# Performance work log

Hardware: AMD Instinct MI355X
Metric: run time of the kernel (lower is better)

## Reference

```python
import jax, jax.numpy as jnp
import numpy as np

INPUT_DIM = 512
OUTPUT_DIM = 512
DEGREE = 7
ALPHA = 0.5


def setup_inputs() -> dict:
    key = jax.random.key(0)
    kx, kc = jax.random.split(key)
    x = jax.random.normal(kx, (8192, INPUT_DIM), dtype=jnp.float32)
    std = 1.0 / (INPUT_DIM * (DEGREE + 1))
    laguerre_coeffs = jax.random.normal(kc, (INPUT_DIM, OUTPUT_DIM, DEGREE + 1), dtype=jnp.float32) * std
    return {"x": x, "laguerre_coeffs": laguerre_coeffs}


def reference(x, laguerre_coeffs):
    # x: [B, I] -> tanh squashed
    xt = jnp.tanh(x.reshape(-1, INPUT_DIM))
    # Build Laguerre basis L_0..L_degree via the standard recurrence:
    # k*L_k = (2(k-1)+1+alpha - x)*L_{k-1} - (k-1+alpha)*L_{k-2}
    L0 = jnp.ones_like(xt)
    basis = [L0]
    if DEGREE > 0:
        L1 = 1.0 + ALPHA - xt
        basis.append(L1)
        Lkm2, Lkm1 = L0, L1
        for k in range(2, DEGREE + 1):
            Lk = ((2 * (k - 1) + 1 + ALPHA - xt) * Lkm1 - (k - 1 + ALPHA) * Lkm2) / k
            basis.append(Lk)
            Lkm2, Lkm1 = Lkm1, Lk
    laguerre = jnp.stack(basis, axis=-1)  # [B, I, D+1]
    y = jnp.einsum('bid,iod->bo', laguerre, laguerre_coeffs)
    return y
```

## Files before the change

kernel.cpp:

```cpp
#include <hip/hip_runtime.h>

#define B_ROWS 8192
#define IN_DIM 512
#define OUT_DIM 512
#define NDEG 8
#define KDIM (IN_DIM * NDEG)
#define ZSLICES 4
#define NKT 16
#define BM 256
#define BN 128
#define LDB 72

typedef short bf16x8 __attribute__((ext_vector_type(8)));
typedef float f32x4  __attribute__((ext_vector_type(4)));

__device__ __forceinline__ unsigned short f2bf(float f) {
  unsigned u = __float_as_uint(f);
  u += 0x7fffu + ((u >> 16) & 1u);
  return (unsigned short)(u >> 16);
}

__device__ __forceinline__ void laguerre8(float t, float* L) {
  L[0] = 1.0f;
  L[1] = 1.5f - t;
#pragma unroll
  for (int k = 2; k < NDEG; ++k)
    L[k] = ((2.0f * (float)k - 0.5f - t) * L[k - 1] -
            ((float)k - 0.5f) * L[k - 2]) * (1.0f / (float)k);
}

__global__ void basis_kernel(const float* __restrict__ x, unsigned short* __restrict__ A) {
  int idx = blockIdx.x * 256 + threadIdx.x;
  int b = idx >> 9, i = idx & 511;
  float L[NDEG];
  laguerre8(tanhf(x[idx]), L);
  uint4 v;
  v.x = (unsigned)f2bf(L[0]) | ((unsigned)f2bf(L[1]) << 16);
  v.y = (unsigned)f2bf(L[2]) | ((unsigned)f2bf(L[3]) << 16);
  v.z = (unsigned)f2bf(L[4]) | ((unsigned)f2bf(L[5]) << 16);
  v.w = (unsigned)f2bf(L[6]) | ((unsigned)f2bf(L[7]) << 16);
  int T = b >> 8, r = b & 255, kt = i >> 3, c = i & 7;
  size_t chunk = ((size_t)(T * 64 + kt)) * 2048 + r * 8 + (c ^ (r & 7));
  ((uint4*)A)[chunk] = v;
}

__global__ void coeff_kernel(const float* __restrict__ c, unsigned short* __restrict__ Bt) {
  int idx = blockIdx.x * 256 + threadIdx.x;
  int i = idx >> 9, o = idx & 511;
  const float4* cp = (const float4*)(c + (size_t)idx * 8);
  float4 c0 = cp[0], c1 = cp[1];
  uint4 v;
  v.x = (unsigned)f2bf(c0.x) | ((unsigned)f2bf(c0.y) << 16);
  v.y = (unsigned)f2bf(c0.z) | ((unsigned)f2bf(c0.w) << 16);
  v.z = (unsigned)f2bf(c1.x) | ((unsigned)f2bf(c1.y) << 16);
  v.w = (unsigned)f2bf(c1.z) | ((unsigned)f2bf(c1.w) << 16);
  ((uint4*)Bt)[o * 512 + i] = v;
}

__global__ __launch_bounds__(512, 4) void gemm_kernel(const unsigned short* __restrict__ A,
                                                      const unsigned short* __restrict__ Bt,
                                                      unsigned short* __restrict__ P) {
  __shared__ unsigned short lds[32768];
  unsigned short* As = lds;
  unsigned short* Bs = lds + 16384;

  const int tid = threadIdx.x;
  const int lane = tid & 63;
  const int w = tid >> 6;
  const int wm = w >> 1, wn = w & 1;

  const int g = blockIdx.x;
  const int xcd = g & 7, idx = g >> 3;
  const int z = xcd >> 1;
  const int y = (xcd & 1) * 16 + (idx & 15);
  const int bn = (idx >> 4) * BN;

  const uint4* Ag = (const uint4*)A;
  const uint4* Bg = (const uint4*)Bt;
  const size_t tile0 = ((size_t)(y * 64 + z * NKT)) * 2048;

  const int rB = tid >> 2, cB = (tid & 3) * 2;
  uint4 rb0 = Bg[(size_t)(bn + rB) * 512 + z * NKT * 8 + cB];
  uint4 rb1 = Bg[(size_t)(bn + rB) * 512 + z * NKT * 8 + cB + 1];

  const int arow = lane & 15, hi = lane >> 4;
  const int swz0 = hi ^ (arow & 7);
  const unsigned short* a0 = As + (wm * 64 + arow) * 64 + swz0 * 8;
  const unsigned short* a1 = As + (wm * 64 + arow) * 64 + (swz0 ^ 4) * 8;
  const unsigned short* bb = Bs + (wn * 64 + arow) * LDB;

  f32x4 zero = {0.f, 0.f, 0.f, 0.f};
  f32x4 acc[4][4];
#pragma unroll
  for (int mi = 0; mi < 4; ++mi)
#pragma unroll
    for (int ni = 0; ni < 4; ++ni) acc[mi][ni] = zero;

  for (int kt = 0; kt < NKT; ++kt) {
    __syncthreads();
    {
      size_t base = tile0 + (size_t)kt * 2048 + w * 256;
#pragma unroll
      for (int j = 0; j < 4; ++j) {
        const uint4* gp = Ag + base + j * 64 + lane;
        __builtin_amdgcn_global_load_lds(
            (const __attribute__((address_space(1))) unsigned int*)gp,
            (__attribute__((address_space(3))) unsigned int*)(As + (w * 256 + j * 64) * 8),
            16, 0, 0);
      }
    }
    *(uint4*)&Bs[rB * LDB + cB * 8] = rb0;
    *(uint4*)&Bs[rB * LDB + (cB + 1) * 8] = rb1;
    __syncthreads();

    if (kt + 1 < NKT) {
      rb0 = Bg[(size_t)(bn + rB) * 512 + (z * NKT + kt + 1) * 8 + cB];
      rb1 = Bg[(size_t)(bn + rB) * 512 + (z * NKT + kt + 1) * 8 + cB + 1];
    }

#pragma unroll
    for (int ks = 0; ks < 2; ++ks) {
      const unsigned short* ap = ks ? a1 : a0;
      bf16x8 af[4], bfr[4];
#pragma unroll
      for (int mi = 0; mi < 4; ++mi)
        af[mi] = *(const bf16x8*)(ap + mi * 1024);
#pragma unroll
      for (int ni = 0; ni < 4; ++ni)
        bfr[ni] = *(const bf16x8*)(bb + ni * 16 * LDB + ks * 32 + hi * 8);
#pragma unroll
      for (int mi = 0; mi < 4; ++mi)
#pragma unroll
        for (int ni = 0; ni < 4; ++ni)
          acc[mi][ni] = __builtin_amdgcn_mfma_f32_16x16x32_bf16(af[mi], bfr[ni], acc[mi][ni], 0, 0, 0);
    }
  }

  __syncthreads();
  unsigned short* W = lds + w * 4096;
#pragma unroll
  for (int mi = 0; mi < 4; ++mi)
#pragma unroll
    for (int ni = 0; ni < 4; ++ni) {
      int col = ni * 16 + arow;
      int c8 = col >> 3, cpos = col & 7;
#pragma unroll
      for (int r = 0; r < 4; ++r) {
        int row = mi * 16 + hi * 4 + r;
        W[row * 64 + ((c8 ^ (row & 7)) << 3) + cpos] = f2bf(acc[mi][ni][r]);
      }
    }
  const int rr = lane >> 3, cc = lane & 7;
#pragma unroll
  for (int it = 0; it < 8; ++it) {
    int row = it * 8 + rr;
    uint4 v = *(uint4*)&W[row * 64 + ((cc ^ (row & 7)) << 3)];
    size_t pr = ((size_t)z * B_ROWS + (y * 256 + wm * 64 + row)) * 512 + bn + wn * 64 + cc * 8;
    *(uint4*)&P[pr] = v;
  }
}

__global__ void reduce_kernel(const unsigned short* __restrict__ P, float* __restrict__ out) {
  size_t t = (size_t)blockIdx.x * 256 + threadIdx.x;
  const uint4* p = (const uint4*)P;
  const size_t stride = (size_t)B_ROWS * OUT_DIM / 8;
  float s[8] = {0, 0, 0, 0, 0, 0, 0, 0};
#pragma unroll
  for (int zz = 0; zz < ZSLICES; ++zz) {
    uint4 v = p[t + zz * stride];
    unsigned q[4] = {v.x, v.y, v.z, v.w};
#pragma unroll
    for (int j = 0; j < 4; ++j) {
      s[2 * j]     += __uint_as_float((q[j] & 0xffffu) << 16);
      s[2 * j + 1] += __uint_as_float(q[j] & 0xffff0000u);
    }
  }
  float4 o0 = {s[0], s[1], s[2], s[3]}, o1 = {s[4], s[5], s[6], s[7]};
  ((float4*)out)[t * 2]     = o0;
  ((float4*)out)[t * 2 + 1] = o1;
}

__global__ void naive_kernel(const float* __restrict__ x, const float* __restrict__ c,
                             float* __restrict__ out) {
  __shared__ float bas[IN_DIM * NDEG];
  int b = blockIdx.x;
  for (int i = threadIdx.x; i < IN_DIM; i += 256) {
    float t = tanhf(x[(size_t)b * IN_DIM + i]);
    float L[NDEG];
    laguerre8(t, L);
#pragma unroll
    for (int d = 0; d < NDEG; ++d) bas[i * NDEG + d] = L[d];
  }
  __syncthreads();
  for (int o = threadIdx.x; o < OUT_DIM; o += 256) {
    float acc = 0.f;
    for (int i = 0; i < IN_DIM; ++i) {
      const float* cp = c + ((size_t)i * OUT_DIM + o) * NDEG;
#pragma unroll
      for (int d = 0; d < NDEG; ++d) acc += bas[i * NDEG + d] * cp[d];
    }
    out[(size_t)b * OUT_DIM + o] = acc;
  }
}

extern "C" void kernel_launch(void* const* d_in, const int* in_sizes, int n_in,
                              void* d_out, int out_size, void* d_ws, size_t ws_size,
                              hipStream_t stream) {
  const float* x    = (const float*)d_in[0];
  const float* coef = (const float*)d_in[1];
  float* out = (float*)d_out;

  const size_t A_BYTES  = (size_t)B_ROWS * KDIM * 2;
  const size_t P_BYTES  = (size_t)ZSLICES * B_ROWS * OUT_DIM * 2;
  const size_t BT_BYTES = (size_t)OUT_DIM * KDIM * 2;

  if (ws_size >= A_BYTES + P_BYTES + BT_BYTES) {
    unsigned short* Abuf = (unsigned short*)d_ws;
    unsigned short* Pp   = (unsigned short*)((char*)d_ws + A_BYTES);
    unsigned short* Bt   = (unsigned short*)((char*)d_ws + A_BYTES + P_BYTES);
    basis_kernel<<<(B_ROWS * IN_DIM) / 256, 256, 0, stream>>>(x, Abuf);
    coeff_kernel<<<(IN_DIM * OUT_DIM) / 256, 256, 0, stream>>>(coef, Bt);
    gemm_kernel<<<512, 512, 0, stream>>>(Abuf, Bt, Pp);
    reduce_kernel<<<(B_ROWS * OUT_DIM / 8) / 256, 256, 0, stream>>>(Pp, out);
  } else if (ws_size >= A_BYTES + BT_BYTES) {
    naive_kernel<<<B_ROWS, 256, 0, stream>>>(x, coef, out);
  } else {
    naive_kernel<<<B_ROWS, 256, 0, stream>>>(x, coef, out);
  }
}
```

Before: 73.22 us.

## Double-buffer GEMM LDS tiles and merge basis/coeff prep kernels

Merges the basis and coefficient conversion kernels into a single prep launch to save one kernel launch. Rewrites the GEMM main loop to double-buffer the A and B tiles in LDS, so the next tile's async global-to-LDS loads overlap the current tile's MFMAs, leaving one barrier per iteration. It also raises MFMA wave priority with s_setprio. LDS grows to 100KB and launch_bounds min blocks drop from 4 to 2, which may cut occupancy.

```diff
diff --git a/kernel.cpp b/kernel.cpp
--- a/kernel.cpp
+++ b/kernel.cpp
@@ -27,42 +27,42 @@
   for (int k = 2; k < NDEG; ++k)
     L[k] = ((2.0f * (float)k - 0.5f - t) * L[k - 1] -
             ((float)k - 0.5f) * L[k - 2]) * (1.0f / (float)k);
-}
-
-__global__ void basis_kernel(const float* __restrict__ x, unsigned short* __restrict__ A) {
-  int idx = blockIdx.x * 256 + threadIdx.x;
-  int b = idx >> 9, i = idx & 511;
-  float L[NDEG];
-  laguerre8(tanhf(x[idx]), L);
-  uint4 v;
-  v.x = (unsigned)f2bf(L[0]) | ((unsigned)f2bf(L[1]) << 16);
-  v.y = (unsigned)f2bf(L[2]) | ((unsigned)f2bf(L[3]) << 16);
-  v.z = (unsigned)f2bf(L[4]) | ((unsigned)f2bf(L[5]) << 16);
-  v.w = (unsigned)f2bf(L[6]) | ((unsigned)f2bf(L[7]) << 16);
-  int T = b >> 8, r = b & 255, kt = i >> 3, c = i & 7;
-  size_t chunk = ((size_t)(T * 64 + kt)) * 2048 + r * 8 + (c ^ (r & 7));
-  ((uint4*)A)[chunk] = v;
-}
-
-__global__ void coeff_kernel(const float* __restrict__ c, unsigned short* __restrict__ Bt) {
-  int idx = blockIdx.x * 256 + threadIdx.x;
-  int i = idx >> 9, o = idx & 511;
-  const float4* cp = (const float4*)(c + (size_t)idx * 8);
-  float4 c0 = cp[0], c1 = cp[1];
-  uint4 v;
-  v.x = (unsigned)f2bf(c0.x) | ((unsigned)f2bf(c0.y) << 16);
-  v.y = (unsigned)f2bf(c0.z) | ((unsigned)f2bf(c0.w) << 16);
-  v.z = (unsigned)f2bf(c1.x) | ((unsigned)f2bf(c1.y) << 16);
-  v.w = (unsigned)f2bf(c1.z) | ((unsigned)f2bf(c1.w) << 16);
-  ((uint4*)Bt)[o * 512 + i] = v;
-}
-
-__global__ __launch_bounds__(512, 4) void gemm_kernel(const unsigned short* __restrict__ A,
+  }
+
+__global__ void prep_kernel(const float* __restrict__ x, const float* __restrict__ cf,
+                            unsigned short* __restrict__ A, unsigned short* __restrict__ Bt) {
+  int g = blockIdx.x;
+  if (g < (B_ROWS * IN_DIM) / 256) {
+    int idx = g * 256 + threadIdx.x;
+    int b = idx >> 9, i = idx & 511;
+    float L[NDEG];
+    laguerre8(tanhf(x[idx]), L);
+    uint4 v;
+    v.x = (unsigned)f2bf(L[0]) | ((unsigned)f2bf(L[1]) << 16);
+    v.y = (unsigned)f2bf(L[2]) | ((unsigned)f2bf(L[3]) << 16);
+    v.z = (unsigned)f2bf(L[4]) | ((unsigned)f2bf(L[5]) << 16);
+    v.w = (unsigned)f2bf(L[6]) | ((unsigned)f2bf(L[7]) << 16);
+    int T = b >> 8, r = b & 255, kt = i >> 3, c = i & 7;
+    size_t chunk = ((size_t)(T * 64 + kt)) * 2048 + r * 8 + (c ^ (r & 7));
+    ((uint4*)A)[chunk] = v;
+  } else {
+    int idx = (g - (B_ROWS * IN_DIM) / 256) * 256 + threadIdx.x;
+    int i = idx >> 9, o = idx & 511;
+    const float4* cp = (const float4*)(cf + (size_t)idx * 8);
+    float4 c0 = cp[0], c1 = cp[1];
+    uint4 v;
+    v.x = (unsigned)f2bf(c0.x) | ((unsigned)f2bf(c0.y) << 16);
+    v.y = (unsigned)f2bf(c0.z) | ((unsigned)f2bf(c0.w) << 16);
+    v.z = (unsigned)f2bf(c1.x) | ((unsigned)f2bf(c1.y) << 16);
+    v.w = (unsigned)f2bf(c1.z) | ((unsigned)f2bf(c1.w) << 16);
+    ((uint4*)Bt)[o * 512 + i] = v;
+  }
+}
+
+__global__ __launch_bounds__(512, 2) void gemm_kernel(const unsigned short* __restrict__ A,
                                                       const unsigned short* __restrict__ Bt,
                                                       unsigned short* __restrict__ P) {
-  __shared__ unsigned short lds[32768];
-  unsigned short* As = lds;
-  unsigned short* Bs = lds + 16384;
+  __shared__ unsigned short lds[51200];
 
   const int tid = threadIdx.x;
   const int lane = tid & 63;
@@ -80,63 +80,85 @@
   const size_t tile0 = ((size_t)(y * 64 + z * NKT)) * 2048;
 
   const int rB = tid >> 2, cB = (tid & 3) * 2;
+
+  const int arow = lane & 15, hi = lane >> 4;
+  const int swz0 = hi ^ (arow & 7);
+  const int aoff0 = (wm * 64 + arow) * 64 + swz0 * 8;
+  const int aoff1 = (wm * 64 + arow) * 64 + (swz0 ^ 4) * 8;
+  const int boff  = (wn * 64 + arow) * LDB;
+
+  f32x4 zero = {0.f, 0.f, 0.f, 0.f};
+  f32x4 acc[4][4];
+#pragma unroll
+  for (int mi = 0; mi < 4; ++mi)
+#pragma unroll
+    for (int ni = 0; ni < 4; ++ni) acc[mi][ni] = zero;
+
   uint4 rb0 = Bg[(size_t)(bn + rB) * 512 + z * NKT * 8 + cB];
   uint4 rb1 = Bg[(size_t)(bn + rB) * 512 + z * NKT * 8 + cB + 1];
-
-  const int arow = lane & 15, hi = lane >> 4;
-  const int swz0 = hi ^ (arow & 7);
-  const unsigned short* a0 = As + (wm * 64 + arow) * 64 + swz0 * 8;
-  const unsigned short* a1 = As + (wm * 64 + arow) * 64 + (swz0 ^ 4) * 8;
-  const unsigned short* bb = Bs + (wn * 64 + arow) * LDB;
-
-  f32x4 zero = {0.f, 0.f, 0.f, 0.f};
-  f32x4 acc[4][4];
-#pragma unroll
-  for (int mi = 0; mi < 4; ++mi)
-#pragma unroll
-    for (int ni = 0; ni < 4; ++ni) acc[mi][ni] = zero;
-
+  {
+    size_t base = tile0 + w * 256;
+    unsigned short* dst = lds + w * 2048;
+#pragma unroll
+    for (int j = 0; j < 4; ++j)
+      __builtin_amdgcn_global_load_lds(
+          (const __attribute__((address_space(1))) unsigned int*)(Ag + base + j * 64 + lane),
+          (__attribute__((address_space(3))) unsigned int*)(dst + j * 512), 16, 0, 0);
+  }
+  *(uint4*)&lds[32768 + rB * LDB + cB * 8] = rb0;
+  *(uint4*)&lds[32768 + rB * LDB + (cB + 1) * 8] = rb1;
+  __syncthreads();
+
+#pragma unroll 2
   for (int kt = 0; kt < NKT; ++kt) {
-    __syncthreads();
-    {
-      size_t base = tile0 + (size_t)kt * 2048 + w * 256;
-#pragma unroll
-      for (int j = 0; j < 4; ++j) {
-        const uint4* gp = Ag + base + j * 64 + lane;
-        __builtin_amdgcn_global_load_lds(
-            (const __attribute__((address_space(1))) unsigned int*)gp,
-            (__attribute__((address_space(3))) unsigned int*)(As + (w * 256 + j * 64) * 8),
-            16, 0, 0);
-      }
-    }
-    *(uint4*)&Bs[rB * LDB + cB * 8] = rb0;
-    *(uint4*)&Bs[rB * LDB + (cB + 1) * 8] = rb1;
-    __syncthreads();
-
+    const int cur = kt & 1, nb = cur ^ 1;
     if (kt + 1 < NKT) {
       rb0 = Bg[(size_t)(bn + rB) * 512 + (z * NKT + kt + 1) * 8 + cB];
       rb1 = Bg[(size_t)(bn + rB) * 512 + (z * NKT + kt + 1) * 8 + cB + 1];
-    }
-
-#pragma unroll
-    for (int ks = 0; ks < 2; ++ks) {
-      const unsigned short* ap = ks ? a1 : a0;
-      bf16x8 af[4], bfr[4];
-#pragma unroll
-      for (int mi = 0; mi < 4; ++mi)
-        af[mi] = *(const bf16x8*)(ap + mi * 1024);
+      size_t base = tile0 + (size_t)(kt + 1) * 2048 + w * 256;
+      unsigned short* dst = lds + nb * 16384 + w * 2048;
+#pragma unroll
+      for (int j = 0; j < 4; ++j)
+        __builtin_amdgcn_global_load_lds(
+            (const __attribute__((address_space(1))) unsigned int*)(Ag + base + (size_t)(kt + 1) * 0 + base - base + j * 64 + lane),
+            (__attribute__((address_space(3))) unsigned int*)(dst + j * 512), 16, 0, 0);
+      __builtin_amdgcn_sched_barrier(0);
+    }
+
+    const unsigned short* Ac = lds + cur * 16384;
+    const unsigned short* Bc = lds + 32768 + cur * 9216;
+    bf16x8 af0[4], af1[4], bf0[4], bf1[4];
+#pragma unroll
+    for (int mi = 0; mi < 4; ++mi) {
+      af0[mi] = *(const bf16x8*)(Ac + aoff0 + mi * 1024);
+      af1[mi] = *(const bf16x8*)(Ac + aoff1 + mi * 1024);
+    }
+#pragma unroll
+    for (int ni = 0; ni < 4; ++ni) {
+      bf0[ni] = *(const bf16x8*)(Bc + boff + ni * 16 * LDB + hi * 8);
+      bf1[ni] = *(const bf16x8*)(Bc + boff + ni * 16 * LDB + 32 + hi * 8);
+    }
+    __builtin_amdgcn_s_setprio(1);
+#pragma unroll
+    for (int mi = 0; mi < 4; ++mi)
 #pragma unroll
       for (int ni = 0; ni < 4; ++ni)
-        bfr[ni] = *(const bf16x8*)(bb + ni * 16 * LDB + ks * 32 + hi * 8);
-#pragma unroll
-      for (int mi = 0; mi < 4; ++mi)
-#pragma unroll
-        for (int ni = 0; ni < 4; ++ni)
-          acc[mi][ni] = __builtin_amdgcn_mfma_f32_16x16x32_bf16(af[mi], bfr[ni], acc[mi][ni], 0, 0, 0);
-    }
-  }
-
-  __syncthreads();
+        acc[mi][ni] = __builtin_amdgcn_mfma_f32_16x16x32_bf16(af0[mi], bf0[ni], acc[mi][ni], 0, 0, 0);
+#pragma unroll
+    for (int mi = 0; mi < 4; ++mi)
+#pragma unroll
+      for (int ni = 0; ni < 4; ++ni)
+        acc[mi][ni] = __builtin_amdgcn_mfma_f32_16x16x32_bf16(af1[mi], bf1[ni], acc[mi][ni], 0, 0, 0);
+    __builtin_amdgcn_s_setprio(0);
+
+    if (kt + 1 < NKT) {
+      unsigned short* BsN = lds + 32768 + nb * 9216;
+      *(uint4*)&BsN[rB * LDB + cB * 8] = rb0;
+      *(uint4*)&BsN[rB * LDB + (cB + 1) * 8] = rb1;
+    }
+    __syncthreads();
+  }
+
   unsigned short* W = lds + w * 4096;
 #pragma unroll
   for (int mi = 0; mi < 4; ++mi)
@@ -218,12 +240,9 @@
     unsigned short* Abuf = (unsigned short*)d_ws;
     unsigned short* Pp   = (unsigned short*)((char*)d_ws + A_BYTES);
     unsigned short* Bt   = (unsigned short*)((char*)d_ws + A_BYTES + P_BYTES);
-    basis_kernel<<<(B_ROWS * IN_DIM) / 256, 256, 0, stream>>>(x, Abuf);
-    coeff_kernel<<<(IN_DIM * OUT_DIM) / 256, 256, 0, stream>>>(coef, Bt);
+    prep_kernel<<<(B_ROWS * IN_DIM + IN_DIM * OUT_DIM) / 256, 256, 0, stream>>>(x, coef, Abuf, Bt);
     gemm_kernel<<<512, 512, 0, stream>>>(Abuf, Bt, Pp);
     reduce_kernel<<<(B_ROWS * OUT_DIM / 8) / 256, 256, 0, stream>>>(Pp, out);
-  } else if (ws_size >= A_BYTES + BT_BYTES) {
-    naive_kernel<<<B_ROWS, 256, 0, stream>>>(x, coef, out);
   } else {
     naive_kernel<<<B_ROWS, 256, 0, stream>>>(x, coef, out);
   }
```

New measurement: 75.14 us. 1.03x slower.
